# Optimization experiments

Hardware: AMD Instinct MI355X
Metric: run time of the kernel (lower is better)

The kernel has to match this reference:

```python
import jax, jax.numpy as jnp
import numpy as np

B, T, C, H = 8, 4096, 384, 64

def setup_inputs() -> dict:
    key = jax.random.key(0)
    k1, k2, k3, k4 = jax.random.split(key, 4)
    x = jax.random.normal(k1, (B, T, C), dtype=jnp.float32)
    # nn.Linear(C, H, bias=False) weight applied as x @ W (W stored [C, H])
    s = 1.0 / np.sqrt(C)
    Wk = jax.random.normal(k2, (C, H), dtype=jnp.float32) * s
    Wq = jax.random.normal(k3, (C, H), dtype=jnp.float32) * s
    Wv = jax.random.normal(k4, (C, H), dtype=jnp.float32) * s
    return {"x": x, "Wk": Wk, "Wq": Wq, "Wv": Wv}

def reference(x, Wk, Wq, Wv):
    Bx, Tx, Cx = x.shape
    k = x @ Wk  # [B,T,H]
    q = x @ Wq  # [B,T,H]
    v = x @ Wv  # [B,T,H]
    # NOTE: original scales by C**-0.5 (embedding dim), not head_size**-0.5
    w = jnp.einsum('bth,bsh->bts', q, k) * (Cx ** -0.5)  # [B,T,T]
    causal = jnp.tril(jnp.ones((Tx, Tx), dtype=bool))
    w = jnp.where(causal, w, -jnp.inf)
    w = jax.nn.softmax(w, axis=-1)
    # dropout omitted (eval mode / deterministic reference)
    out = jnp.einsum('bts,bsh->bth', w, v)  # [B,T,H]
    return out
```

## Files before the change

### kernel.cpp

```cpp
#include <hip/hip_runtime.h>
#include <hip/hip_bf16.h>


typedef __bf16 bf16x8 __attribute__((ext_vector_type(8)));
typedef float  f32x4  __attribute__((ext_vector_type(4)));

#define BB   8
#define TT   4096
#define CC   384
#define HH   64
#define NROW (BB*TT)
#define QSCALE (0.05103103630798288f * 1.4426950408889634f)

#if __has_builtin(__builtin_amdgcn_exp2f)
#define EXP2(x) __builtin_amdgcn_exp2f(x)
#else
#define EXP2(x) exp2f(x)
#endif

__device__ __forceinline__ unsigned short f2bf(float f) {
    __bf16 h = (__bf16)f;
    return __builtin_bit_cast(unsigned short, h);
}

__global__ __launch_bounds__(256) void wtrans_kernel(
        const float* __restrict__ Wk,
        const float* __restrict__ Wq,
        const float* __restrict__ Wv,
        unsigned short* __restrict__ Wt) {
    __shared__ __align__(16) unsigned short tile[64][72];
    const float* Wm = (blockIdx.y == 0) ? Wk : ((blockIdx.y == 1) ? Wq : Wv);
    unsigned short* Wtm = Wt + blockIdx.y * (HH * CC);
    const int c0 = blockIdx.x * 64;
#pragma unroll
    for (int i = 0; i < 16; ++i) {
        int id = threadIdx.x + i * 256;
        int c = id >> 6, h = id & 63;
        tile[c][h] = f2bf(Wm[(c0 + c) * HH + h]);
    }
    __syncthreads();
#pragma unroll
    for (int i = 0; i < 16; ++i) {
        int id = threadIdx.x + i * 256;
        int h = id >> 6, c = id & 63;
        Wtm[h * CC + c0 + c] = tile[c][h];
    }
}

__global__ __launch_bounds__(256, 1) void qkv_kernel(
        const float* __restrict__ x,
        const unsigned short* __restrict__ Wt,
        unsigned short* __restrict__ q_ws,
        unsigned short* __restrict__ k_ws,
        unsigned short* __restrict__ vt_ws) {
    __shared__ __align__(16) float xs[6][32][64];
    __shared__ __align__(16) unsigned short vtile[64][40];

    const int lane = threadIdx.x & 63;
    const int wv   = threadIdx.x >> 6;
    const int rt   = wv & 1;
    const int hh   = wv >> 1;
    const int l15  = lane & 15;
    const int quad = lane >> 4;
    const int rb   = blockIdx.x * 32;
    const int ntb  = hh * 2;

#pragma unroll
    for (int kk = 0; kk < 6; ++kk) {
#pragma unroll
        for (int j = 0; j < 2; ++j) {
            const int r0 = wv * 8 + j * 4;
            const int r  = r0 + quad;
            const int ch = l15 ^ (r & 7);
            const float* src = x + (long)(rb + r) * CC + kk * 64 + ch * 4;
            float* dst = &xs[kk][r0][0];
            __builtin_amdgcn_global_load_lds(
                (const __attribute__((address_space(1))) unsigned int*)src,
                (__attribute__((address_space(3))) unsigned int*)dst,
                16, 0, 0);
        }
    }

    bf16x8 bf[2][12];
    auto loadW = [&](int kk, bf16x8* dst) {
#pragma unroll
        for (int m = 0; m < 3; ++m)
#pragma unroll
            for (int n = 0; n < 2; ++n)
#pragma unroll
                for (int h01 = 0; h01 < 2; ++h01)
                    dst[m * 4 + n * 2 + h01] = *reinterpret_cast<const bf16x8*>(
                        Wt + m * (HH * CC) + ((ntb + n) * 16 + l15) * CC
                          + kk * 64 + h01 * 32 + quad * 8);
    };
    loadW(0, bf[0]);

    f32x4 acc[3][2];
    const f32x4 zero = {0.f, 0.f, 0.f, 0.f};
#pragma unroll
    for (int m = 0; m < 3; ++m)
#pragma unroll
        for (int n = 0; n < 2; ++n) acc[m][n] = zero;

    const int rloc = rt * 16 + l15;
    const int rx7  = rloc & 7;

    __asm volatile("s_waitcnt vmcnt(0)" ::: "memory");
    __syncthreads();

#pragma unroll
    for (int kk = 0; kk < 6; ++kk) {
        if (kk < 5) {
            loadW(kk + 1, bf[(kk + 1) & 1]);
            __asm volatile("" ::: "memory");
        }
#pragma unroll
        for (int h01 = 0; h01 < 2; ++h01) {
            const int chb = 8 * h01 + 2 * quad;
            const f32x4 xa = *reinterpret_cast<const f32x4*>(
                &xs[kk][rloc][((chb) ^ rx7) * 4]);
            const f32x4 xb = *reinterpret_cast<const f32x4*>(
                &xs[kk][rloc][((chb + 1) ^ rx7) * 4]);
            bf16x8 a;
#pragma unroll
            for (int e = 0; e < 4; ++e) {
                a[e]     = (__bf16)xa[e];
                a[4 + e] = (__bf16)xb[e];
            }
#pragma unroll
            for (int m = 0; m < 3; ++m)
#pragma unroll
                for (int n = 0; n < 2; ++n)
                    acc[m][n] = __builtin_amdgcn_mfma_f32_16x16x32_bf16(
                        a, bf[kk & 1][m * 4 + n * 2 + h01], acc[m][n], 0, 0, 0);
        }
    }

#pragma unroll
    for (int n = 0; n < 2; ++n) {
        const int nt = ntb + n;
        const int h  = nt * 16 + l15;
        const int c8 = h >> 3;
        const int jj = h & 7;
#pragma unroll
        for (int r = 0; r < 4; ++r) {
            const int gr = rb + rt * 16 + quad * 4 + r;
            const int s   = gr & 63;
            const int stp = ((s >> 4) & 2) + ((s >> 2) & 1);
            const int ip  = ((s >> 1) & 12) + (s & 3);
            k_ws[(long)(gr >> 6) * 4096 + stp * 1024 + c8 * 128 + ip * 8 + jj]
                = f2bf(acc[0][n][r]);
            q_ws[gr * HH + h] = f2bf(acc[1][n][r] * QSCALE);
            vtile[h][rt * 16 + quad * 4 + r] = f2bf(acc[2][n][r]);
        }
    }
    __syncthreads();
    {
        const int id  = threadIdx.x;
        const int dt  = id >> 6, scl = (id >> 4) & 3, ii = id & 15;
        const int sc  = scl + ((rb >> 3) & 4);
        unsigned short* dst = vt_ws + (long)(rb >> 6) * 4096
                              + (dt * 8 + sc) * 128 + ii * 8;
        *reinterpret_cast<uint4*>(dst) =
            *reinterpret_cast<const uint4*>(&vtile[dt * 16 + ii][scl * 8]);
    }
}

__global__ __launch_bounds__(1024, 4) void attn_kernel(
        const unsigned short* __restrict__ q_ws,
        const unsigned short* __restrict__ k_ws,
        const unsigned short* __restrict__ vt_ws,
        float* __restrict__ out) {
    __shared__ __align__(16) float xchg[64 * 65];
    __shared__ float mx1[64], lx1[64];

    const int lane = threadIdx.x & 63;
    const int wv16 = threadIdx.x >> 6;
    const int grp  = wv16 >> 2;
    const int wg   = wv16 & 3;
    const int l15  = lane & 15;
    const int quad = lane >> 4;

    const int bid = blockIdx.x;
    const int b   = bid & 7;
    const int p   = bid >> 3;

    const f32x4 zero = {0.f, 0.f, 0.f, 0.f};

    auto do_tile = [&](int t, int qt, int qrow,
                       const bf16x8& qf0, const bf16x8& qf1,
                       f32x4* o, float& mprev, float& lsum) {
        const int s0 = t * 64;
        const unsigned short* ktile = k_ws + ((long)((b * TT + s0) >> 4)) * 1024;
        const unsigned short* vtile = vt_ws + ((long)((b * TT + s0) >> 6)) * 4096;

        bf16x8 ka0[4], ka1[4];
#pragma unroll
        for (int st = 0; st < 4; ++st) {
            ka0[st] = *reinterpret_cast<const bf16x8*>(
                ktile + ((st * 8 + quad) * 16 + l15) * 8);
            ka1[st] = *reinterpret_cast<const bf16x8*>(
                ktile + ((st * 8 + 4 + quad) * 16 + l15) * 8);
        }
        bf16x8 vb0[4], vb1[4];
#pragma unroll
        for (int dt = 0; dt < 4; ++dt) {
            vb0[dt] = *reinterpret_cast<const bf16x8*>(
                vtile + dt * 1024 + quad * 128 + l15 * 8);
            vb1[dt] = *reinterpret_cast<const bf16x8*>(
                vtile + dt * 1024 + (4 + quad) * 128 + l15 * 8);
        }

        f32x4 sc[4];
        __builtin_amdgcn_s_setprio(1);
#pragma unroll
        for (int st = 0; st < 4; ++st) {
            f32x4 z = zero;
            z = __builtin_amdgcn_mfma_f32_16x16x32_bf16(ka0[st], qf0, z, 0, 0, 0);
            z = __builtin_amdgcn_mfma_f32_16x16x32_bf16(ka1[st], qf1, z, 0, 0, 0);
            sc[st] = z;
        }
        __builtin_amdgcn_s_setprio(0);

        if (t == qt) {
#pragma unroll
            for (int st = 0; st < 4; ++st)
#pragma unroll
                for (int r = 0; r < 4; ++r) {
                    int sg = s0 + ((st >> 1) << 5) + (quad << 3)
                               + ((st & 1) << 2) + r;
                    if (sg > qrow) sc[st][r] = -1e30f;
                }
        }

        float mloc = -1e30f;
#pragma unroll
        for (int st = 0; st < 4; ++st)
#pragma unroll
            for (int r = 0; r < 4; ++r) mloc = fmaxf(mloc, sc[st][r]);
        mloc = fmaxf(mloc, __shfl_xor(mloc, 16));
        mloc = fmaxf(mloc, __shfl_xor(mloc, 32));

        if (!__all(mloc <= mprev + 8.0f)) {
            const float mnew = fmaxf(mprev, mloc);
            const float alpha = EXP2(mprev - mnew);
            lsum *= alpha;
            float ar[4];
#pragma unroll
            for (int r = 0; r < 4; ++r) ar[r] = __shfl(alpha, quad * 4 + r);
#pragma unroll
            for (int dt = 0; dt < 4; ++dt)
#pragma unroll
                for (int r = 0; r < 4; ++r) o[dt][r] *= ar[r];
            mprev = mnew;
        }

        float psum = 0.f;
#pragma unroll
        for (int st = 0; st < 4; ++st)
#pragma unroll
            for (int r = 0; r < 4; ++r) {
                float pv = EXP2(sc[st][r] - mprev);
                psum += pv;
                sc[st][r] = pv;
            }
        lsum += psum;

        bf16x8 pf0, pf1;
#pragma unroll
        for (int r = 0; r < 4; ++r) {
            pf0[r]     = (__bf16)sc[0][r];
            pf0[4 + r] = (__bf16)sc[1][r];
            pf1[r]     = (__bf16)sc[2][r];
            pf1[4 + r] = (__bf16)sc[3][r];
        }
        __builtin_amdgcn_s_setprio(1);
#pragma unroll
        for (int dt = 0; dt < 4; ++dt) {
            o[dt] = __builtin_amdgcn_mfma_f32_16x16x32_bf16(pf0, vb0[dt], o[dt], 0, 0, 0);
            o[dt] = __builtin_amdgcn_mfma_f32_16x16x32_bf16(pf1, vb1[dt], o[dt], 0, 0, 0);
        }
        __builtin_amdgcn_s_setprio(0);
    };

    auto merge_store = [&](int qt, f32x4* o, float& mprev, float& lsum) {
        lsum += __shfl_xor(lsum, 16);
        lsum += __shfl_xor(lsum, 32);
        for (int rr = 1; rr < 4; ++rr) {
            __syncthreads();
            if (grp == rr) {
                if (quad == 0) { mx1[wg * 16 + l15] = mprev; lx1[wg * 16 + l15] = lsum; }
#pragma unroll
                for (int dt = 0; dt < 4; ++dt)
#pragma unroll
                    for (int r = 0; r < 4; ++r)
                        xchg[(wg * 16 + quad * 4 + r) * 65 + dt * 16 + l15] = o[dt][r];
            }
            __syncthreads();
            if (grp == 0) {
#pragma unroll
                for (int r = 0; r < 4; ++r) {
                    const int row = wg * 16 + quad * 4 + r;
                    const float m0r = __shfl(mprev, quad * 4 + r);
                    const float m1r = mx1[row];
                    const float ms  = fmaxf(m0r, m1r);
                    const float w0  = EXP2(m0r - ms);
                    const float w1  = EXP2(m1r - ms);
#pragma unroll
                    for (int dt = 0; dt < 4; ++dt)
                        o[dt][r] = o[dt][r] * w0 + xchg[row * 65 + dt * 16 + l15] * w1;
                }
                const float m1l = mx1[wg * 16 + l15];
                const float msl = fmaxf(mprev, m1l);
                lsum = EXP2(mprev - msl) * lsum + EXP2(m1l - msl) * lx1[wg * 16 + l15];
                mprev = msl;
            }
        }
        if (grp == 0) {
            float rl[4];
#pragma unroll
            for (int r = 0; r < 4; ++r) rl[r] = 1.0f / __shfl(lsum, quad * 4 + r);
            const int orow = qt * 64 + wg * 16 + quad * 4;
#pragma unroll
            for (int dt = 0; dt < 4; ++dt)
#pragma unroll
                for (int r = 0; r < 4; ++r)
                    out[(long)(b * TT + orow + r) * HH + dt * 16 + l15] = o[dt][r] * rl[r];
        }
        __syncthreads();
    };

    {
        const int qt = 63 - p;
        const int qrow = qt * 64 + wg * 16 + l15;
        const unsigned short* qbase = q_ws + (b * TT + qrow) * HH;
        const bf16x8 qf0 = *reinterpret_cast<const bf16x8*>(qbase + quad * 8);
        const bf16x8 qf1 = *reinterpret_cast<const bf16x8*>(qbase + 32 + quad * 8);
        f32x4 o[4];
#pragma unroll
        for (int dt = 0; dt < 4; ++dt) o[dt] = zero;
        float mprev = -1e30f, lsum = 0.f;
        for (int t = grp; t <= qt; t += 4)
            do_tile(t, qt, qrow, qf0, qf1, o, mprev, lsum);
        merge_store(qt, o, mprev, lsum);
    }

    {
        const int qt = p;
        const int qrow = qt * 64 + wg * 16 + l15;
        const unsigned short* qbase = q_ws + (b * TT + qrow) * HH;
        const bf16x8 qf0 = *reinterpret_cast<const bf16x8*>(qbase + quad * 8);
        const bf16x8 qf1 = *reinterpret_cast<const bf16x8*>(qbase + 32 + quad * 8);
        f32x4 o[4];
#pragma unroll
        for (int dt = 0; dt < 4; ++dt) o[dt] = zero;
        float mprev = -1e30f, lsum = 0.f;
        for (int t = grp; t <= qt; t += 4)
            do_tile(t, qt, qrow, qf0, qf1, o, mprev, lsum);
        merge_store(qt, o, mprev, lsum);
    }
}

extern "C" void kernel_launch(void* const* d_in, const int* in_sizes, int n_in,
                              void* d_out, int out_size, void* d_ws, size_t ws_size,
                              hipStream_t stream) {
    const float* x  = (const float*)d_in[0];
    const float* Wk = (const float*)d_in[1];
    const float* Wq = (const float*)d_in[2];
    const float* Wv = (const float*)d_in[3];
    float* out = (float*)d_out;

    char* ws = (char*)d_ws;
    unsigned short* Wt    = (unsigned short*)(ws);
    unsigned short* q_ws  = (unsigned short*)(ws + 147456);
    unsigned short* k_ws  = (unsigned short*)(ws + 147456 + 4194304);
    unsigned short* vt_ws = (unsigned short*)(ws + 147456 + 2 * 4194304);

    wtrans_kernel<<<dim3(6, 3), 256, 0, stream>>>(Wk, Wq, Wv, Wt);
    qkv_kernel<<<NROW / 32, 256, 0, stream>>>(x, Wt, q_ws, k_ws, vt_ws);
    attn_kernel<<<(TT / 128) * BB, 1024, 0, stream>>>(q_ws, k_ws, vt_ws, out);
}
```

Before: 160.3 us.

## Split attention into one query tile per 512-thread block with 2-way KV split

Each attention block now handles a single 64-row query tile with two wave groups splitting the KV tiles, instead of pairing tiles qt and 63-qt in a 1024-thread block with a 4-way KV split. The grid doubles to 512 blocks and the merge becomes one exchange step rather than three. This cuts intra-block synchronization and merge overhead and gives the scheduler more, smaller blocks. The cost is losing the paired-tile load balancing, so block durations now vary with causal length.

```diff
diff --git a/kernel.cpp b/kernel.cpp
--- a/kernel.cpp
+++ b/kernel.cpp
@@ -166,7 +166,7 @@
     }
 }
 
-__global__ __launch_bounds__(1024, 4) void attn_kernel(
+__global__ __launch_bounds__(512, 4) void attn_kernel(
         const unsigned short* __restrict__ q_ws,
         const unsigned short* __restrict__ k_ws,
         const unsigned short* __restrict__ vt_ws,
@@ -175,19 +175,19 @@
     __shared__ float mx1[64], lx1[64];
 
     const int lane = threadIdx.x & 63;
-    const int wv16 = threadIdx.x >> 6;
-    const int grp  = wv16 >> 2;
-    const int wg   = wv16 & 3;
+    const int wv8  = threadIdx.x >> 6;
+    const int grp  = wv8 >> 2;
+    const int wg   = wv8 & 3;
     const int l15  = lane & 15;
     const int quad = lane >> 4;
 
     const int bid = blockIdx.x;
     const int b   = bid & 7;
-    const int p   = bid >> 3;
+    const int qt  = 63 - (bid >> 3);
 
     const f32x4 zero = {0.f, 0.f, 0.f, 0.f};
 
-    auto do_tile = [&](int t, int qt, int qrow,
+    auto do_tile = [&](int t, int qrow,
                        const bf16x8& qf0, const bf16x8& qf1,
                        f32x4* o, float& mprev, float& lsum) {
         const int s0 = t * 64;
@@ -283,55 +283,7 @@
         __builtin_amdgcn_s_setprio(0);
     };
 
-    auto merge_store = [&](int qt, f32x4* o, float& mprev, float& lsum) {
-        lsum += __shfl_xor(lsum, 16);
-        lsum += __shfl_xor(lsum, 32);
-        for (int rr = 1; rr < 4; ++rr) {
-            __syncthreads();
-            if (grp == rr) {
-                if (quad == 0) { mx1[wg * 16 + l15] = mprev; lx1[wg * 16 + l15] = lsum; }
-#pragma unroll
-                for (int dt = 0; dt < 4; ++dt)
-#pragma unroll
-                    for (int r = 0; r < 4; ++r)
-                        xchg[(wg * 16 + quad * 4 + r) * 65 + dt * 16 + l15] = o[dt][r];
-            }
-            __syncthreads();
-            if (grp == 0) {
-#pragma unroll
-                for (int r = 0; r < 4; ++r) {
-                    const int row = wg * 16 + quad * 4 + r;
-                    const float m0r = __shfl(mprev, quad * 4 + r);
-                    const float m1r = mx1[row];
-                    const float ms  = fmaxf(m0r, m1r);
-                    const float w0  = EXP2(m0r - ms);
-                    const float w1  = EXP2(m1r - ms);
-#pragma unroll
-                    for (int dt = 0; dt < 4; ++dt)
-                        o[dt][r] = o[dt][r] * w0 + xchg[row * 65 + dt * 16 + l15] * w1;
-                }
-                const float m1l = mx1[wg * 16 + l15];
-                const float msl = fmaxf(mprev, m1l);
-                lsum = EXP2(mprev - msl) * lsum + EXP2(m1l - msl) * lx1[wg * 16 + l15];
-                mprev = msl;
-            }
-        }
-        if (grp == 0) {
-            float rl[4];
-#pragma unroll
-            for (int r = 0; r < 4; ++r) rl[r] = 1.0f / __shfl(lsum, quad * 4 + r);
-            const int orow = qt * 64 + wg * 16 + quad * 4;
-#pragma unroll
-            for (int dt = 0; dt < 4; ++dt)
-#pragma unroll
-                for (int r = 0; r < 4; ++r)
-                    out[(long)(b * TT + orow + r) * HH + dt * 16 + l15] = o[dt][r] * rl[r];
-        }
-        __syncthreads();
-    };
-
     {
-        const int qt = 63 - p;
         const int qrow = qt * 64 + wg * 16 + l15;
         const unsigned short* qbase = q_ws + (b * TT + qrow) * HH;
         const bf16x8 qf0 = *reinterpret_cast<const bf16x8*>(qbase + quad * 8);
@@ -340,24 +292,49 @@
 #pragma unroll
         for (int dt = 0; dt < 4; ++dt) o[dt] = zero;
         float mprev = -1e30f, lsum = 0.f;
-        for (int t = grp; t <= qt; t += 4)
-            do_tile(t, qt, qrow, qf0, qf1, o, mprev, lsum);
-        merge_store(qt, o, mprev, lsum);
-    }
-
-    {
-        const int qt = p;
-        const int qrow = qt * 64 + wg * 16 + l15;
-        const unsigned short* qbase = q_ws + (b * TT + qrow) * HH;
-        const bf16x8 qf0 = *reinterpret_cast<const bf16x8*>(qbase + quad * 8);
-        const bf16x8 qf1 = *reinterpret_cast<const bf16x8*>(qbase + 32 + quad * 8);
-        f32x4 o[4];
-#pragma unroll
-        for (int dt = 0; dt < 4; ++dt) o[dt] = zero;
-        float mprev = -1e30f, lsum = 0.f;
-        for (int t = grp; t <= qt; t += 4)
-            do_tile(t, qt, qrow, qf0, qf1, o, mprev, lsum);
-        merge_store(qt, o, mprev, lsum);
+        for (int t = grp; t <= qt; t += 2)
+            do_tile(t, qrow, qf0, qf1, o, mprev, lsum);
+
+        lsum += __shfl_xor(lsum, 16);
+        lsum += __shfl_xor(lsum, 32);
+
+        __syncthreads();
+        if (grp == 1) {
+            if (quad == 0) { mx1[wg * 16 + l15] = mprev; lx1[wg * 16 + l15] = lsum; }
+#pragma unroll
+            for (int dt = 0; dt < 4; ++dt)
+#pragma unroll
+                for (int r = 0; r < 4; ++r)
+                    xchg[(wg * 16 + quad * 4 + r) * 65 + dt * 16 + l15] = o[dt][r];
+        }
+        __syncthreads();
+        if (grp == 0) {
+#pragma unroll
+            for (int r = 0; r < 4; ++r) {
+                const int row = wg * 16 + quad * 4 + r;
+                const float m0r = __shfl(mprev, quad * 4 + r);
+                const float m1r = mx1[row];
+                const float ms  = fmaxf(m0r, m1r);
+                const float w0  = EXP2(m0r - ms);
+                const float w1  = EXP2(m1r - ms);
+#pragma unroll
+                for (int dt = 0; dt < 4; ++dt)
+                    o[dt][r] = o[dt][r] * w0 + xchg[row * 65 + dt * 16 + l15] * w1;
+            }
+            const float m1l = mx1[wg * 16 + l15];
+            const float msl = fmaxf(mprev, m1l);
+            lsum = EXP2(mprev - msl) * lsum + EXP2(m1l - msl) * lx1[wg * 16 + l15];
+
+            float rl[4];
+#pragma unroll
+            for (int r = 0; r < 4; ++r) rl[r] = 1.0f / __shfl(lsum, quad * 4 + r);
+            const int orow = qt * 64 + wg * 16 + quad * 4;
+#pragma unroll
+            for (int dt = 0; dt < 4; ++dt)
+#pragma unroll
+                for (int r = 0; r < 4; ++r)
+                    out[(long)(b * TT + orow + r) * HH + dt * 16 + l15] = o[dt][r] * rl[r];
+        }
     }
 }
 
@@ -378,5 +355,5 @@
 
     wtrans_kernel<<<dim3(6, 3), 256, 0, stream>>>(Wk, Wq, Wv, Wt);
     qkv_kernel<<<NROW / 32, 256, 0, stream>>>(x, Wt, q_ws, k_ws, vt_ws);
-    attn_kernel<<<(TT / 128) * BB, 1024, 0, stream>>>(q_ws, k_ws, vt_ws, out);
-}
+    attn_kernel<<<(TT / 64) * BB, 512, 0, stream>>>(q_ws, k_ws, vt_ws, out);
+}
```

Result: slower. 170.3 us (+6.3%).

## Double-buffer x and W tiles in LDS for the QKV projection kernel

Applied to the files above, without the earlier changes.

Replaces the up-front staging of all six x chunks plus per-wave register prefetch of W with a two-stage LDS double buffer. Both x and the bf16 transposed weights are loaded asynchronously via global_load_lds, and W fragments are read from a swizzled LDS tile. This shrinks the LDS footprint and shares W across waves instead of each wave loading its own copy. In exchange it adds a vmcnt wait and barrier on every k-step, plus extra LDS reads inside the MFMA loop.

```diff
diff --git a/kernel.cpp b/kernel.cpp
--- a/kernel.cpp
+++ b/kernel.cpp
@@ -53,7 +53,8 @@
         unsigned short* __restrict__ q_ws,
         unsigned short* __restrict__ k_ws,
         unsigned short* __restrict__ vt_ws) {
-    __shared__ __align__(16) float xs[6][32][64];
+    __shared__ __align__(16) float xs2[2][32][64];
+    __shared__ __align__(16) unsigned short wts[2][3][64][64];
     __shared__ __align__(16) unsigned short vtile[64][40];
 
     const int lane = threadIdx.x & 63;
@@ -65,35 +66,38 @@
     const int rb   = blockIdx.x * 32;
     const int ntb  = hh * 2;
 
-#pragma unroll
-    for (int kk = 0; kk < 6; ++kk) {
+    auto stageX = [&](int kk, int bb) {
 #pragma unroll
         for (int j = 0; j < 2; ++j) {
             const int r0 = wv * 8 + j * 4;
             const int r  = r0 + quad;
             const int ch = l15 ^ (r & 7);
             const float* src = x + (long)(rb + r) * CC + kk * 64 + ch * 4;
-            float* dst = &xs[kk][r0][0];
+            float* dst = &xs2[bb][r0][0];
             __builtin_amdgcn_global_load_lds(
                 (const __attribute__((address_space(1))) unsigned int*)src,
                 (__attribute__((address_space(3))) unsigned int*)dst,
                 16, 0, 0);
         }
-    }
-
-    bf16x8 bf[2][12];
-    auto loadW = [&](int kk, bf16x8* dst) {
-#pragma unroll
-        for (int m = 0; m < 3; ++m)
-#pragma unroll
-            for (int n = 0; n < 2; ++n)
-#pragma unroll
-                for (int h01 = 0; h01 < 2; ++h01)
-                    dst[m * 4 + n * 2 + h01] = *reinterpret_cast<const bf16x8*>(
-                        Wt + m * (HH * CC) + ((ntb + n) * 16 + l15) * CC
-                          + kk * 64 + h01 * 32 + quad * 8);
     };
-    loadW(0, bf[0]);
+
+    auto stageW = [&](int kk, int bb) {
+#pragma unroll
+        for (int i = 0; i < 6; ++i) {
+            const int j   = wv + 4 * i;
+            const int m   = j >> 3;
+            const int rg  = j & 7;
+            const int h   = rg * 8 + (lane >> 3);
+            const int chs = (lane & 7) ^ (h & 7);
+            const unsigned short* src =
+                Wt + m * (HH * CC) + h * CC + kk * 64 + chs * 8;
+            unsigned short* dst = &wts[bb][m][rg * 8][0];
+            __builtin_amdgcn_global_load_lds(
+                (const __attribute__((address_space(1))) unsigned int*)src,
+                (__attribute__((address_space(3))) unsigned int*)dst,
+                16, 0, 0);
+        }
+    };
 
     f32x4 acc[3][2];
     const f32x4 zero = {0.f, 0.f, 0.f, 0.f};
@@ -104,23 +108,24 @@
 
     const int rloc = rt * 16 + l15;
     const int rx7  = rloc & 7;
-
+    const int hx7  = l15 & 7;
+
+    stageX(0, 0);
+    stageW(0, 0);
     __asm volatile("s_waitcnt vmcnt(0)" ::: "memory");
     __syncthreads();
 
 #pragma unroll
     for (int kk = 0; kk < 6; ++kk) {
-        if (kk < 5) {
-            loadW(kk + 1, bf[(kk + 1) & 1]);
-            __asm volatile("" ::: "memory");
-        }
+        const int cur = kk & 1;
+        if (kk < 5) { stageX(kk + 1, cur ^ 1); stageW(kk + 1, cur ^ 1); }
 #pragma unroll
         for (int h01 = 0; h01 < 2; ++h01) {
             const int chb = 8 * h01 + 2 * quad;
             const f32x4 xa = *reinterpret_cast<const f32x4*>(
-                &xs[kk][rloc][((chb) ^ rx7) * 4]);
+                &xs2[cur][rloc][((chb) ^ rx7) * 4]);
             const f32x4 xb = *reinterpret_cast<const f32x4*>(
-                &xs[kk][rloc][((chb + 1) ^ rx7) * 4]);
+                &xs2[cur][rloc][((chb + 1) ^ rx7) * 4]);
             bf16x8 a;
 #pragma unroll
             for (int e = 0; e < 4; ++e) {
@@ -130,10 +135,16 @@
 #pragma unroll
             for (int m = 0; m < 3; ++m)
 #pragma unroll
-                for (int n = 0; n < 2; ++n)
+                for (int n = 0; n < 2; ++n) {
+                    const int hN = (ntb + n) * 16 + l15;
+                    const bf16x8 bfr = *reinterpret_cast<const bf16x8*>(
+                        &wts[cur][m][hN][(((h01 << 2) + quad) ^ hx7) << 3]);
                     acc[m][n] = __builtin_amdgcn_mfma_f32_16x16x32_bf16(
-                        a, bf[kk & 1][m * 4 + n * 2 + h01], acc[m][n], 0, 0, 0);
-        }
+                        a, bfr, acc[m][n], 0, 0, 0);
+                }
+        }
+        __asm volatile("s_waitcnt vmcnt(0)" ::: "memory");
+        __syncthreads();
     }
 
 #pragma unroll
```

After: 139.2 us. 1.15x faster.
